# Optimization experiments

Measured on AMD Instinct MI355X. Metric: run time of the kernel, lower is better.

## Reference

```python
import jax, jax.numpy as jnp
import numpy as np

EPS_DEN = 1e-7
EPS_SQRT = 1e-12  # clamp before sqrt (torch.cdist matmul-mode also clamps at 0)


def setup_inputs() -> dict:
    key = jax.random.key(0)
    k1, k2 = jax.random.split(key)
    L, N, Q, C = 6, 256, 64, 256
    hs_pair = jax.random.normal(k1, (L, N, Q, C), dtype=jnp.float32)
    centers = jax.random.normal(k2, (L, N, 2, C), dtype=jnp.float32)
    return {"hs_pair": hs_pair, "centers": centers}


def reference(hs_pair, centers):
    # hs_pair: [L, N, Q, C], centers: [L, N, 2, C]
    L, N, Q, C = hs_pair.shape
    x2 = jnp.sum(hs_pair * hs_pair, axis=-1)  # [L, N, Q], constant over iters

    def body(carry, _):
        cen, _prev_a = carry
        c2 = jnp.sum(cen * cen, axis=-1)                     # [L, N, 2]
        xc = jnp.einsum('lnqc,lnkc->lnqk', hs_pair, cen)     # [L, N, Q, 2]
        d2 = x2[..., None] + c2[:, :, None, :] - 2.0 * xc
        dist = jnp.sqrt(jnp.maximum(d2, EPS_SQRT))           # euclidean cdist
        a = jax.nn.softmax(-dist, axis=-1)                   # [L, N, Q, 2]
        num = jnp.einsum('lnqk,lnqc->lnkc', a, hs_pair)      # [L, N, 2, C]
        den = jnp.sum(a, axis=2)                             # [L, N, 2]
        new_cen = num / (den[..., None] + EPS_DEN)
        return (new_cen, a), None

    init_a = jnp.zeros((L, N, Q, 2), dtype=hs_pair.dtype)
    # Q sequential EM iterations; final assignment is the one computed from
    # the centers *before* the last update (matches the torch loop order).
    (centers_out, assignment), _ = jax.lax.scan(body, (centers, init_a), None, length=Q)
    return centers_out, assignment
```

## Files before the change

kernel.cpp:

```cpp
#include <hip/hip_runtime.h>

namespace {
constexpr int PB = 6 * 256;
constexpr int Q = 64;
constexpr int C = 256;
constexpr float EPS_DEN = 1e-7f;
constexpr float EPS_SQRT = 1e-12f;
constexpr int GT_FLOATS = Q * Q;
constexpr int AUX_FLOATS = 256;

typedef __attribute__((ext_vector_type(8))) short bf16x8;
typedef __attribute__((ext_vector_type(4))) float f32x4;

template <int CTRL>
__device__ __forceinline__ float ror_add(float v) {
  int r = __builtin_amdgcn_mov_dpp(__float_as_int(v), CTRL, 0xF, 0xF, true);
  return v + __int_as_float(r);
}

__device__ __forceinline__ float wave_total(float v) {
  v = ror_add<0x121>(v);
  v = ror_add<0x122>(v);
  v = ror_add<0x124>(v);
  v = ror_add<0x128>(v);
  {
    int t = __builtin_amdgcn_update_dpp(0, __float_as_int(v), 0x142, 0xA, 0xF,
                                        true);
    v = v + __int_as_float(t);
  }
  {
    int t = __builtin_amdgcn_update_dpp(0, __float_as_int(v), 0x143, 0xC, 0xF,
                                        true);
    v = v + __int_as_float(t);
  }
  return __int_as_float(__builtin_amdgcn_readlane(__float_as_int(v), 63));
}

__device__ __forceinline__ ushort bf16_rne(float x) {
  uint u = __float_as_uint(x);
  return (ushort)((u + 0x7FFFu + ((u >> 16) & 1u)) >> 16);
}
__device__ __forceinline__ float bf16_up(ushort h) {
  return __uint_as_float((uint)h << 16);
}

__device__ __forceinline__ void cvt8(float4 x, float4 y, bf16x8& hh,
                                     bf16x8& ll) {
  float v[8] = {x.x, x.y, x.z, x.w, y.x, y.y, y.z, y.w};
#pragma unroll
  for (int j = 0; j < 8; ++j) {
    ushort h = bf16_rne(v[j]);
    hh[j] = (short)h;
    ll[j] = (short)bf16_rne(v[j] - bf16_up(h));
  }
}

__device__ __forceinline__ void gload_lds16(const float* src, float* lds_dst) {
  __builtin_amdgcn_global_load_lds(
      (const __attribute__((address_space(1))) unsigned int*)src,
      (__attribute__((address_space(3))) unsigned int*)lds_dst, 16, 0, 0);
}

__device__ __forceinline__ void wave_fence() { asm volatile("" ::: "memory"); }
}

__global__ __launch_bounds__(256, 2) void k1_gram(
    const float* __restrict__ hs, const float* __restrict__ cen,
    float* __restrict__ ws) {
  const int prob = blockIdx.x;
  const int tid = threadIdx.x;
  const int lane = tid & 63, w = tid >> 6;
  const int li = lane & 15, lk = lane >> 4;

  __shared__ __align__(16) float Fq[64 * 64];

  const float* __restrict__ hsb = hs + (size_t)prob * Q * C;
  const float* __restrict__ cenb = cen + (size_t)prob * 2 * C;
  float* gtp = ws + (size_t)prob * GT_FLOATS;
  float* aux = ws + (size_t)PB * GT_FLOATS + (size_t)prob * AUX_FLOATS;

  {
    float c0v = cenb[tid];
    float c1v = cenb[C + tid];
    float p0 = wave_total(c0v * c0v);
    float p1 = wave_total(c1v * c1v);
    if (lane == 0) {
      aux[192 + w] = p0;
      aux[196 + w] = p1;
    }
  }

  f32x4 acc[4] = {{0.f, 0.f, 0.f, 0.f},
                  {0.f, 0.f, 0.f, 0.f},
                  {0.f, 0.f, 0.f, 0.f},
                  {0.f, 0.f, 0.f, 0.f}};
  f32x4 accX = {0.f, 0.f, 0.f, 0.f};
  const int rA = 16 * w + li;

#pragma unroll 1
  for (int q = 0; q < 4; ++q) {
#pragma unroll
    for (int i = 0; i < 4; ++i) {
      const int j = w * 4 + i;
      const int r = 4 * j + (lane >> 4);
      const int hg = lane & 15;
      const float* src =
          hsb + r * C + q * 64 + ((hg ^ ((r & 7) << 1)) << 2);
      gload_lds16(src, Fq + j * 256);
    }
    __syncthreads();

#pragma unroll
    for (int kk2 = 0; kk2 < 2; ++kk2) {
      const int kk = q * 2 + kk2;
      const int hg0 = kk2 * 8 + lk * 2;
      bf16x8 ah, al;
      {
        float4 f0 = *(const float4*)&Fq[rA * 64 + ((hg0 ^ ((rA & 7) << 1)) << 2)];
        float4 f1 =
            *(const float4*)&Fq[rA * 64 + (((hg0 + 1) ^ ((rA & 7) << 1)) << 2)];
        cvt8(f0, f1, ah, al);
      }
      bf16x8 cbh = {0, 0, 0, 0, 0, 0, 0, 0};
      bf16x8 cbl = {0, 0, 0, 0, 0, 0, 0, 0};
      if (li < 2) {
        const float* pc = cenb + li * C + kk * 32 + lk * 8;
        cvt8(*(const float4*)pc, *(const float4*)(pc + 4), cbh, cbl);
      }
      accX = __builtin_amdgcn_mfma_f32_16x16x32_bf16(ah, cbh, accX, 0, 0, 0);
      accX = __builtin_amdgcn_mfma_f32_16x16x32_bf16(ah, cbl, accX, 0, 0, 0);
      accX = __builtin_amdgcn_mfma_f32_16x16x32_bf16(al, cbh, accX, 0, 0, 0);

#pragma unroll
      for (int tj = 0; tj < 4; ++tj) {
        if (tj < w) continue;
        const int rB = 16 * tj + li;
        float4 g0 =
            *(const float4*)&Fq[rB * 64 + ((hg0 ^ ((rB & 7) << 1)) << 2)];
        float4 g1 =
            *(const float4*)&Fq[rB * 64 + (((hg0 + 1) ^ ((rB & 7) << 1)) << 2)];
        bf16x8 bh, bl;
        cvt8(g0, g1, bh, bl);
        acc[tj] =
            __builtin_amdgcn_mfma_f32_16x16x32_bf16(ah, bh, acc[tj], 0, 0, 0);
        acc[tj] =
            __builtin_amdgcn_mfma_f32_16x16x32_bf16(ah, bl, acc[tj], 0, 0, 0);
        acc[tj] =
            __builtin_amdgcn_mfma_f32_16x16x32_bf16(al, bh, acc[tj], 0, 0, 0);
      }
    }
    __syncthreads();
  }

#pragma unroll
  for (int tj = 0; tj < 4; ++tj) {
    if (tj < w) continue;
#pragma unroll
    for (int r = 0; r < 4; ++r) {
      const float v = acc[tj][r];
      const int row = 16 * w + lk * 4 + r;
      const int col = 16 * tj + li;
      gtp[(col >> 2) * 256 + row * 4 + (col & 3)] = v;
      if (tj > w) gtp[(row >> 2) * 256 + col * 4 + (row & 3)] = v;
      if (row == col) aux[128 + row] = v;
    }
  }
  if (li < 2) {
#pragma unroll
    for (int r = 0; r < 4; ++r) {
      const int q = 16 * w + lk * 4 + r;
      aux[q * 2 + li] = accX[r];
    }
  }
}

__global__ __launch_bounds__(64, 2) void k2_iter(const float* __restrict__ hs,
                                                 const float* __restrict__ ws,
                                                 float* __restrict__ out) {
  const int prob = blockIdx.x;
  const int lane = threadIdx.x;
  const int li = lane & 15, lk = lane >> 4;

  __shared__ __align__(16) ushort Ah[2][64];
  __shared__ __align__(16) float m_s[2][64];
  __shared__ __align__(16) float a_s[2 * Q];

  const float4* gt4 = (const float4*)(ws + (size_t)prob * GT_FLOATS);
  const float* aux = ws + (size_t)PB * GT_FLOATS + (size_t)prob * AUX_FLOATS;

  bf16x8 Gh[4][2], Gl[4][2];
#pragma unroll
  for (int t = 0; t < 4; ++t) {
#pragma unroll
    for (int kk = 0; kk < 2; ++kk) {
      const int cj = 8 * kk + 2 * lk;
      float4 ga = gt4[cj * 64 + 16 * t + li];
      float4 gb = gt4[(cj + 1) * 64 + 16 * t + li];
      float g[8] = {ga.x, ga.y, ga.z, ga.w, gb.x, gb.y, gb.z, gb.w};
      bf16x8 hh, ll;
#pragma unroll
      for (int j = 0; j < 8; ++j) {
        ushort h = bf16_rne(g[j]);
        hh[j] = (short)h;
        ll[j] = (short)bf16_rne(g[j] - bf16_up(h));
      }
      Gh[t][kk] = hh;
      Gl[t][kk] = ll;
    }
  }

  const float x2 = aux[128 + lane];
  float xc0 = aux[lane * 2 + 0];
  float xc1 = aux[lane * 2 + 1];
  float c20 = aux[192] + aux[193] + aux[194] + aux[195];
  float c21 = aux[196] + aux[197] + aux[198] + aux[199];

  float a0 = 0.f, a1 = 0.f;
  const int cl = li & 1;

#pragma unroll 1
  for (int t = 0; t < Q; ++t) {
    float d0 = fmaxf(x2 + c20 - 2.f * xc0, EPS_SQRT);
    float d1 = fmaxf(x2 + c21 - 2.f * xc1, EPS_SQRT);
    float t0 = __builtin_amdgcn_sqrtf(d0), t1 = __builtin_amdgcn_sqrtf(d1);
    float e0 = __expf(-t0), e1 = __expf(-t1);
    float inv = __builtin_amdgcn_rcpf(e0 + e1);
    a0 = e0 * inv;
    a1 = e1 * inv;
    if (t == Q - 1) break;

    Ah[0][lane] = bf16_rne(a0);
    Ah[1][lane] = bf16_rne(a1);
    float den0 = wave_total(a0);
    float den1 = wave_total(a1);
    wave_fence();

    bf16x8 bh[2];
#pragma unroll
    for (int kk = 0; kk < 2; ++kk)
      bh[kk] = *(const bf16x8*)&Ah[cl][kk * 32 + lk * 8];

    f32x4 acc[4] = {{0.f, 0.f, 0.f, 0.f},
                    {0.f, 0.f, 0.f, 0.f},
                    {0.f, 0.f, 0.f, 0.f},
                    {0.f, 0.f, 0.f, 0.f}};
#pragma unroll
    for (int tt = 0; tt < 4; ++tt) {
#pragma unroll
      for (int kk = 0; kk < 2; ++kk) {
        acc[tt] = __builtin_amdgcn_mfma_f32_16x16x32_bf16(Gh[tt][kk], bh[kk],
                                                          acc[tt], 0, 0, 0);
        acc[tt] = __builtin_amdgcn_mfma_f32_16x16x32_bf16(Gl[tt][kk], bh[kk],
                                                          acc[tt], 0, 0, 0);
      }
    }
    if (li < 2) {
#pragma unroll
      for (int tt = 0; tt < 4; ++tt)
        *(float4*)&m_s[li][16 * tt + lk * 4] =
            make_float4(acc[tt][0], acc[tt][1], acc[tt][2], acc[tt][3]);
    }
    wave_fence();

    float m0 = m_s[0][lane];
    float m1 = m_s[1][lane];
    float s0 = wave_total(a0 * m0);
    float s1 = wave_total(a1 * m1);

    float i0 = __builtin_amdgcn_rcpf(den0 + EPS_DEN);
    float i1 = __builtin_amdgcn_rcpf(den1 + EPS_DEN);
    xc0 = m0 * i0;
    xc1 = m1 * i1;
    c20 = s0 * i0 * i0;
    c21 = s1 * i1 * i1;
  }

  *(float2*)&a_s[lane * 2] = make_float2(a0, a1);
  float den0 = wave_total(a0);
  float den1 = wave_total(a1);
  wave_fence();
  float i0 = __builtin_amdgcn_rcpf(den0 + EPS_DEN);
  float i1 = __builtin_amdgcn_rcpf(den1 + EPS_DEN);

  const float4* hb4 = (const float4*)(hs + (size_t)prob * Q * C);
  const float2* a2 = (const float2*)a_s;
  float4 n0 = make_float4(0.f, 0.f, 0.f, 0.f);
  float4 n1 = make_float4(0.f, 0.f, 0.f, 0.f);
#pragma unroll 8
  for (int q2 = 0; q2 < Q; ++q2) {
    float4 h = hb4[q2 * 64 + lane];
    float2 aq = a2[q2];
    n0.x = fmaf(aq.x, h.x, n0.x);
    n0.y = fmaf(aq.x, h.y, n0.y);
    n0.z = fmaf(aq.x, h.z, n0.z);
    n0.w = fmaf(aq.x, h.w, n0.w);
    n1.x = fmaf(aq.y, h.x, n1.x);
    n1.y = fmaf(aq.y, h.y, n1.y);
    n1.z = fmaf(aq.y, h.z, n1.z);
    n1.w = fmaf(aq.y, h.w, n1.w);
  }
  float4* outc4 = (float4*)(out + (size_t)prob * 2 * C);
  outc4[lane] = make_float4(n0.x * i0, n0.y * i0, n0.z * i0, n0.w * i0);
  outc4[64 + lane] = make_float4(n1.x * i1, n1.y * i1, n1.z * i1, n1.w * i1);

  float* outa = out + (size_t)PB * 2 * C + (size_t)prob * Q * 2;
  *(float2*)&outa[lane * 2] = make_float2(a0, a1);
}

extern "C" void kernel_launch(void* const* d_in, const int* in_sizes, int n_in,
                              void* d_out, int out_size, void* d_ws,
                              size_t ws_size, hipStream_t stream) {
  const float* hs = (const float*)d_in[0];
  const float* cen = (const float*)d_in[1];
  float* out = (float*)d_out;
  float* ws = (float*)d_ws;
  hipLaunchKernelGGL(k1_gram, dim3(PB), dim3(256), 0, stream, hs, cen, ws);
  hipLaunchKernelGGL(k2_iter, dim3(PB), dim3(64), 0, stream, hs, ws, out);
}
```

Measured before the change: 87.81 us.

## Fuse Gram and EM-iteration kernels into one, keeping Gram matrix in LDS

Merges the Gram-matrix kernel and the iterative EM kernel into a single launch per problem. The Gram matrix and the auxiliary terms now stay in shared memory instead of round-tripping through the global workspace, and the second kernel launch goes away. In exchange, only wave 0 runs the serial 64-iteration loop while the other three waves of each 256-thread block exit. This may reduce occupancy and latency hiding for the iteration phase, since each block now holds more LDS and was launched with 256 threads.

Result: faster. 85.39 us (-2.8%).

```diff
diff --git a/kernel.cpp b/kernel.cpp
--- a/kernel.cpp
+++ b/kernel.cpp
@@ -6,8 +6,6 @@
 constexpr int C = 256;
 constexpr float EPS_DEN = 1e-7f;
 constexpr float EPS_SQRT = 1e-12f;
-constexpr int GT_FLOATS = Q * Q;
-constexpr int AUX_FLOATS = 256;
 
 typedef __attribute__((ext_vector_type(8))) short bf16x8;
 typedef __attribute__((ext_vector_type(4))) float f32x4;
@@ -64,20 +62,22 @@
 __device__ __forceinline__ void wave_fence() { asm volatile("" ::: "memory"); }
 }
 
-__global__ __launch_bounds__(256, 2) void k1_gram(
+__global__ __launch_bounds__(256, 2) void em_fused(
     const float* __restrict__ hs, const float* __restrict__ cen,
-    float* __restrict__ ws) {
+    float* __restrict__ out) {
   const int prob = blockIdx.x;
   const int tid = threadIdx.x;
   const int lane = tid & 63, w = tid >> 6;
   const int li = lane & 15, lk = lane >> 4;
 
-  __shared__ __align__(16) float Fq[64 * 64];
+  __shared__ __align__(16) float Gs[64 * 64];
+  __shared__ __align__(16) float aux_s[256];
+  __shared__ __align__(16) ushort Ahs[2][64];
+  __shared__ __align__(16) float m_s[2][64];
+  __shared__ __align__(16) float a_s[2 * Q];
 
   const float* __restrict__ hsb = hs + (size_t)prob * Q * C;
   const float* __restrict__ cenb = cen + (size_t)prob * 2 * C;
-  float* gtp = ws + (size_t)prob * GT_FLOATS;
-  float* aux = ws + (size_t)PB * GT_FLOATS + (size_t)prob * AUX_FLOATS;
 
   {
     float c0v = cenb[tid];
@@ -85,8 +85,8 @@
     float p0 = wave_total(c0v * c0v);
     float p1 = wave_total(c1v * c1v);
     if (lane == 0) {
-      aux[192 + w] = p0;
-      aux[196 + w] = p1;
+      aux_s[192 + w] = p0;
+      aux_s[196 + w] = p1;
     }
   }
 
@@ -104,9 +104,8 @@
       const int j = w * 4 + i;
       const int r = 4 * j + (lane >> 4);
       const int hg = lane & 15;
-      const float* src =
-          hsb + r * C + q * 64 + ((hg ^ ((r & 7) << 1)) << 2);
-      gload_lds16(src, Fq + j * 256);
+      const float* src = hsb + r * C + q * 64 + ((hg ^ ((r & 7) << 1)) << 2);
+      gload_lds16(src, Gs + j * 256);
     }
     __syncthreads();
 
@@ -116,9 +115,10 @@
       const int hg0 = kk2 * 8 + lk * 2;
       bf16x8 ah, al;
       {
-        float4 f0 = *(const float4*)&Fq[rA * 64 + ((hg0 ^ ((rA & 7) << 1)) << 2)];
+        float4 f0 =
+            *(const float4*)&Gs[rA * 64 + ((hg0 ^ ((rA & 7) << 1)) << 2)];
         float4 f1 =
-            *(const float4*)&Fq[rA * 64 + (((hg0 + 1) ^ ((rA & 7) << 1)) << 2)];
+            *(const float4*)&Gs[rA * 64 + (((hg0 + 1) ^ ((rA & 7) << 1)) << 2)];
         cvt8(f0, f1, ah, al);
       }
       bf16x8 cbh = {0, 0, 0, 0, 0, 0, 0, 0};
@@ -136,9 +136,9 @@
         if (tj < w) continue;
         const int rB = 16 * tj + li;
         float4 g0 =
-            *(const float4*)&Fq[rB * 64 + ((hg0 ^ ((rB & 7) << 1)) << 2)];
+            *(const float4*)&Gs[rB * 64 + ((hg0 ^ ((rB & 7) << 1)) << 2)];
         float4 g1 =
-            *(const float4*)&Fq[rB * 64 + (((hg0 + 1) ^ ((rB & 7) << 1)) << 2)];
+            *(const float4*)&Gs[rB * 64 + (((hg0 + 1) ^ ((rB & 7) << 1)) << 2)];
         bf16x8 bh, bl;
         cvt8(g0, g1, bh, bl);
         acc[tj] =
@@ -160,33 +160,23 @@
       const float v = acc[tj][r];
       const int row = 16 * w + lk * 4 + r;
       const int col = 16 * tj + li;
-      gtp[(col >> 2) * 256 + row * 4 + (col & 3)] = v;
-      if (tj > w) gtp[(row >> 2) * 256 + col * 4 + (row & 3)] = v;
-      if (row == col) aux[128 + row] = v;
+      Gs[(col >> 2) * 256 + row * 4 + (col & 3)] = v;
+      if (tj > w) Gs[(row >> 2) * 256 + col * 4 + (row & 3)] = v;
+      if (row == col) aux_s[128 + row] = v;
     }
   }
   if (li < 2) {
 #pragma unroll
     for (int r = 0; r < 4; ++r) {
-      const int q = 16 * w + lk * 4 + r;
-      aux[q * 2 + li] = accX[r];
-    }
-  }
-}
-
-__global__ __launch_bounds__(64, 2) void k2_iter(const float* __restrict__ hs,
-                                                 const float* __restrict__ ws,
-                                                 float* __restrict__ out) {
-  const int prob = blockIdx.x;
-  const int lane = threadIdx.x;
-  const int li = lane & 15, lk = lane >> 4;
-
-  __shared__ __align__(16) ushort Ah[2][64];
-  __shared__ __align__(16) float m_s[2][64];
-  __shared__ __align__(16) float a_s[2 * Q];
-
-  const float4* gt4 = (const float4*)(ws + (size_t)prob * GT_FLOATS);
-  const float* aux = ws + (size_t)PB * GT_FLOATS + (size_t)prob * AUX_FLOATS;
+      const int qq = 16 * w + lk * 4 + r;
+      aux_s[qq * 2 + li] = accX[r];
+    }
+  }
+  __syncthreads();
+
+  if (w != 0) return;
+
+  const float4* gt4 = (const float4*)Gs;
 
   bf16x8 Gh[4][2], Gl[4][2];
 #pragma unroll
@@ -209,11 +199,11 @@
     }
   }
 
-  const float x2 = aux[128 + lane];
-  float xc0 = aux[lane * 2 + 0];
-  float xc1 = aux[lane * 2 + 1];
-  float c20 = aux[192] + aux[193] + aux[194] + aux[195];
-  float c21 = aux[196] + aux[197] + aux[198] + aux[199];
+  const float x2 = aux_s[128 + lane];
+  float xc0 = aux_s[lane * 2 + 0];
+  float xc1 = aux_s[lane * 2 + 1];
+  float c20 = aux_s[192] + aux_s[193] + aux_s[194] + aux_s[195];
+  float c21 = aux_s[196] + aux_s[197] + aux_s[198] + aux_s[199];
 
   float a0 = 0.f, a1 = 0.f;
   const int cl = li & 1;
@@ -229,8 +219,8 @@
     a1 = e1 * inv;
     if (t == Q - 1) break;
 
-    Ah[0][lane] = bf16_rne(a0);
-    Ah[1][lane] = bf16_rne(a1);
+    Ahs[0][lane] = bf16_rne(a0);
+    Ahs[1][lane] = bf16_rne(a1);
     float den0 = wave_total(a0);
     float den1 = wave_total(a1);
     wave_fence();
@@ -238,27 +228,27 @@
     bf16x8 bh[2];
 #pragma unroll
     for (int kk = 0; kk < 2; ++kk)
-      bh[kk] = *(const bf16x8*)&Ah[cl][kk * 32 + lk * 8];
-
-    f32x4 acc[4] = {{0.f, 0.f, 0.f, 0.f},
-                    {0.f, 0.f, 0.f, 0.f},
-                    {0.f, 0.f, 0.f, 0.f},
-                    {0.f, 0.f, 0.f, 0.f}};
+      bh[kk] = *(const bf16x8*)&Ahs[cl][kk * 32 + lk * 8];
+
+    f32x4 macc[4] = {{0.f, 0.f, 0.f, 0.f},
+                     {0.f, 0.f, 0.f, 0.f},
+                     {0.f, 0.f, 0.f, 0.f},
+                     {0.f, 0.f, 0.f, 0.f}};
 #pragma unroll
     for (int tt = 0; tt < 4; ++tt) {
 #pragma unroll
       for (int kk = 0; kk < 2; ++kk) {
-        acc[tt] = __builtin_amdgcn_mfma_f32_16x16x32_bf16(Gh[tt][kk], bh[kk],
-                                                          acc[tt], 0, 0, 0);
-        acc[tt] = __builtin_amdgcn_mfma_f32_16x16x32_bf16(Gl[tt][kk], bh[kk],
-                                                          acc[tt], 0, 0, 0);
+        macc[tt] = __builtin_amdgcn_mfma_f32_16x16x32_bf16(Gh[tt][kk], bh[kk],
+                                                           macc[tt], 0, 0, 0);
+        macc[tt] = __builtin_amdgcn_mfma_f32_16x16x32_bf16(Gl[tt][kk], bh[kk],
+                                                           macc[tt], 0, 0, 0);
       }
     }
     if (li < 2) {
 #pragma unroll
       for (int tt = 0; tt < 4; ++tt)
-        *(float4*)&m_s[li][16 * tt + lk * 4] =
-            make_float4(acc[tt][0], acc[tt][1], acc[tt][2], acc[tt][3]);
+        *(float4*)&m_s[li][16 * tt + lk * 4] = make_float4(
+            macc[tt][0], macc[tt][1], macc[tt][2], macc[tt][3]);
     }
     wave_fence();
 
@@ -282,7 +272,7 @@
   float i0 = __builtin_amdgcn_rcpf(den0 + EPS_DEN);
   float i1 = __builtin_amdgcn_rcpf(den1 + EPS_DEN);
 
-  const float4* hb4 = (const float4*)(hs + (size_t)prob * Q * C);
+  const float4* hb4 = (const float4*)hsb;
   const float2* a2 = (const float2*)a_s;
   float4 n0 = make_float4(0.f, 0.f, 0.f, 0.f);
   float4 n1 = make_float4(0.f, 0.f, 0.f, 0.f);
@@ -313,7 +303,5 @@
   const float* hs = (const float*)d_in[0];
   const float* cen = (const float*)d_in[1];
   float* out = (float*)d_out;
-  float* ws = (float*)d_ws;
-  hipLaunchKernelGGL(k1_gram, dim3(PB), dim3(256), 0, stream, hs, cen, ws);
-  hipLaunchKernelGGL(k2_iter, dim3(PB), dim3(64), 0, stream, hs, ws, out);
-}
+  hipLaunchKernelGGL(em_fused, dim3(PB), dim3(256), 0, stream, hs, cen, out);
+}
```
